# Optimization experiments

Hardware: AMD Instinct MI355X
Metric: run time of the kernel (lower is better)

The kernel has to match this reference:

```python
import jax, jax.numpy as jnp
import numpy as np

BITS = 8
EPS = 1e-5


def round_clip(x, lo, hi):
    # round-then-clip with straight-through estimator (matches Audyn's round_clip)
    return x + jax.lax.stop_gradient(jnp.clip(jnp.round(x), lo, hi) - x)


def setup_inputs() -> dict:
    key = jax.random.key(0)
    kx, kw = jax.random.split(key)
    B, S, D_IN, D_OUT = 4, 2048, 4096, 16384
    x = jax.random.normal(kx, (B, S, D_IN), dtype=jnp.float32)
    # kaiming-uniform-ish scale: bound = 1/sqrt(in_features)
    bound = 1.0 / np.sqrt(D_IN)
    weight = jax.random.uniform(kw, (D_OUT, D_IN), dtype=jnp.float32,
                                minval=-bound, maxval=bound)
    return {"x": x, "weight": weight}


def reference(x, weight):
    q = float(2 ** (BITS - 1))  # 128
    # activation quantization: per-tensor abs-max
    gamma = jnp.maximum(jnp.max(jnp.abs(x)), EPS)
    xq = round_clip(x * (q / gamma), -q, q - 1.0)
    # weight quantization: per-tensor mean-abs (NB: source divides abs_weight, not weight)
    abs_w = jnp.abs(weight)
    beta = jnp.maximum(jnp.mean(abs_w), EPS)
    wq = round_clip(abs_w / beta, -1.0, 1.0)
    # GEMM (no bias: source always registers bias as None) + rescale
    y = jnp.einsum("bsd,od->bso", xq, wq)
    return y * (beta * gamma / q)
```

## Files before the change

### kernel.cpp

```cpp
#include <hip/hip_runtime.h>

typedef float f32x4 __attribute__((ext_vector_type(4)));
typedef int   i32x4 __attribute__((ext_vector_type(4)));
typedef char  s8x16 __attribute__((ext_vector_type(16)));

#define GAS __attribute__((address_space(1)))
#define LAS __attribute__((address_space(3)))

constexpr int M = 8192;
constexpr int N = 16384;
constexpr int K = 4096;
constexpr long long NX = (long long)M * K;
constexpr long long NW = (long long)N * K;
constexpr int NPART = 2048;


__global__ void reduce_absmax_kernel(const float* __restrict__ x,
                                     unsigned* __restrict__ gmax, int n4) {
  float m = 0.f;
  int stride = gridDim.x * blockDim.x;
  for (int i = blockIdx.x * blockDim.x + threadIdx.x; i < n4; i += stride) {
    f32x4 v = *(const f32x4*)(x + (size_t)i * 4);
    m = fmaxf(m, fmaxf(fmaxf(fabsf(v[0]), fabsf(v[1])),
                       fmaxf(fabsf(v[2]), fabsf(v[3]))));
  }
#pragma unroll
  for (int off = 32; off > 0; off >>= 1) m = fmaxf(m, __shfl_down(m, off));
  __shared__ float sm[4];
  int lane = threadIdx.x & 63, wid = threadIdx.x >> 6;
  if (lane == 0) sm[wid] = m;
  __syncthreads();
  if (threadIdx.x == 0) {
    m = fmaxf(fmaxf(sm[0], sm[1]), fmaxf(sm[2], sm[3]));
    atomicMax(gmax, __float_as_uint(m));
  }
}

__global__ void reduce_abssum_kernel(const float* __restrict__ w,
                                     float* __restrict__ partials, int n4) {
  float s = 0.f;
  int stride = gridDim.x * blockDim.x;
  for (int i = blockIdx.x * blockDim.x + threadIdx.x; i < n4; i += stride) {
    f32x4 v = *(const f32x4*)(w + (size_t)i * 4);
    s += fabsf(v[0]) + fabsf(v[1]) + fabsf(v[2]) + fabsf(v[3]);
  }
#pragma unroll
  for (int off = 32; off > 0; off >>= 1) s += __shfl_down(s, off);
  __shared__ float sm[4];
  int lane = threadIdx.x & 63, wid = threadIdx.x >> 6;
  if (lane == 0) sm[wid] = s;
  __syncthreads();
  if (threadIdx.x == 0) partials[blockIdx.x] = (sm[0] + sm[1]) + (sm[2] + sm[3]);
}

__global__ void finalize_kernel(const unsigned* __restrict__ gbits,
                                const float* __restrict__ partials,
                                float* __restrict__ params) {
  __shared__ double sd[256];
  double s = 0.0;
  for (int i = threadIdx.x; i < NPART; i += 256) s += (double)partials[i];
  sd[threadIdx.x] = s;
  __syncthreads();
  for (int h = 128; h > 0; h >>= 1) {
    if (threadIdx.x < h) sd[threadIdx.x] += sd[threadIdx.x + h];
    __syncthreads();
  }
  if (threadIdx.x == 0) {
    float beta  = fmaxf((float)(sd[0] / (double)NW), 1e-5f);
    float gamma = fmaxf(__uint_as_float(gbits[0]), 1e-5f);
    params[0] = 128.0f / gamma;
    params[1] = beta;
    params[2] = beta * gamma / 128.0f;
  }
}


__global__ void quant_x_kernel(const float* __restrict__ x,
                               char* __restrict__ xq,
                               const float* __restrict__ params, int n16) {
  float s = params[0];
  int stride = gridDim.x * blockDim.x;
  for (int i = blockIdx.x * blockDim.x + threadIdx.x; i < n16; i += stride) {
    const f32x4* p = (const f32x4*)(x + (size_t)i * 16);
    s8x16 o;
#pragma unroll
    for (int v = 0; v < 4; ++v) {
      f32x4 t = p[v];
#pragma unroll
      for (int k = 0; k < 4; ++k) {
        float r = fminf(fmaxf(rintf(t[k] * s), -128.f), 127.f);
        o[v * 4 + k] = (char)(int)r;
      }
    }
    *(s8x16*)(xq + (size_t)i * 16) = o;
  }
}

__global__ void quant_w_kernel(const float* __restrict__ w,
                               char* __restrict__ wq,
                               const float* __restrict__ params, int n16) {
  float beta = params[1];
  int stride = gridDim.x * blockDim.x;
  for (int i = blockIdx.x * blockDim.x + threadIdx.x; i < n16; i += stride) {
    const f32x4* p = (const f32x4*)(w + (size_t)i * 16);
    s8x16 o;
#pragma unroll
    for (int v = 0; v < 4; ++v) {
      f32x4 t = p[v];
#pragma unroll
      for (int k = 0; k < 4; ++k) {
        o[v * 4 + k] = (rintf(fabsf(t[k]) / beta) >= 1.0f) ? (char)1 : (char)0;
      }
    }
    *(s8x16*)(wq + (size_t)i * 16) = o;
  }
}


__global__ __launch_bounds__(256) void gemm_kernel(
    const char* __restrict__ A,
    const char* __restrict__ B,
    float* __restrict__ C,
    const float* __restrict__ params) {
  __shared__ __align__(16) char As[128 * 64];
  __shared__ __align__(16) char Bs[128 * 64];

  const int tid  = threadIdx.x;
  const int lane = tid & 63, wid = tid >> 6;
  const int wr = wid >> 1, wc = wid & 1;
  const int r16 = lane & 15, q4 = lane >> 4;
  const int m0 = blockIdx.y * 128, n0 = blockIdx.x * 128;
  const float sc = params[2];

  const int i0 = tid, i1 = 256 + tid;
  const char* ga0 = A + (size_t)(m0 + (i0 >> 2)) * K + (i0 & 3) * 16;
  const char* ga1 = A + (size_t)(m0 + (i1 >> 2)) * K + (i1 & 3) * 16;
  const char* gb0 = B + (size_t)(n0 + (i0 >> 2)) * K + (i0 & 3) * 16;
  const char* gb1 = B + (size_t)(n0 + (i1 >> 2)) * K + (i1 & 3) * 16;
  char* la0 = &As[i0 * 16];
  char* la1 = &As[i1 * 16];
  char* lb0 = &Bs[i0 * 16];
  char* lb1 = &Bs[i1 * 16];

  int aoff[4], boff[4];
#pragma unroll
  for (int i = 0; i < 4; ++i) {
    aoff[i] = (wr * 64 + i * 16 + r16) * 64 + q4 * 16;
    boff[i] = (wc * 64 + i * 16 + r16) * 64 + q4 * 16;
  }

  i32x4 acc[4][4] = {};

  for (int kt = 0; kt < K / 64; ++kt) {
    const int ko = kt * 64;
    __builtin_amdgcn_global_load_lds((const GAS void*)(ga0 + ko), (LAS void*)la0, 16, 0, 0);
    __builtin_amdgcn_global_load_lds((const GAS void*)(ga1 + ko), (LAS void*)la1, 16, 0, 0);
    __builtin_amdgcn_global_load_lds((const GAS void*)(gb0 + ko), (LAS void*)lb0, 16, 0, 0);
    __builtin_amdgcn_global_load_lds((const GAS void*)(gb1 + ko), (LAS void*)lb1, 16, 0, 0);
    __syncthreads();

    i32x4 af[4], bf[4];
#pragma unroll
    for (int i = 0; i < 4; ++i) af[i] = *(const i32x4*)&As[aoff[i]];
#pragma unroll
    for (int j = 0; j < 4; ++j) bf[j] = *(const i32x4*)&Bs[boff[j]];
#pragma unroll
    for (int i = 0; i < 4; ++i)
#pragma unroll
      for (int j = 0; j < 4; ++j)
        acc[i][j] = __builtin_amdgcn_mfma_i32_16x16x64_i8(af[i], bf[j], acc[i][j], 0, 0, 0);
    __syncthreads();
  }

  const int crow = m0 + wr * 64 + q4 * 4;
  const int ccol = n0 + wc * 64 + r16;
#pragma unroll
  for (int i = 0; i < 4; ++i)
#pragma unroll
    for (int j = 0; j < 4; ++j)
#pragma unroll
      for (int r = 0; r < 4; ++r)
        C[(size_t)(crow + i * 16 + r) * N + (ccol + j * 16)] = (float)acc[i][j][r] * sc;
}


extern "C" void kernel_launch(void* const* d_in, const int* in_sizes, int n_in,
                              void* d_out, int out_size, void* d_ws, size_t ws_size,
                              hipStream_t stream) {
  const float* x = (const float*)d_in[0];
  const float* w = (const float*)d_in[1];
  float* out = (float*)d_out;
  char* ws = (char*)d_ws;

  unsigned* gamma_bits = (unsigned*)ws;
  float*    params     = (float*)(ws + 16);
  float*    partials   = (float*)(ws + 256);
  char*     xq = ws + 16384;
  char*     wq = ws + 16384 + (size_t)NX;

  hipMemsetAsync(ws, 0, 256, stream);

  reduce_absmax_kernel<<<NPART, 256, 0, stream>>>(x, gamma_bits, (int)(NX / 4));
  reduce_abssum_kernel<<<NPART, 256, 0, stream>>>(w, partials, (int)(NW / 4));
  finalize_kernel<<<1, 256, 0, stream>>>(gamma_bits, partials, params);
  quant_x_kernel<<<2048, 256, 0, stream>>>(x, xq, params, (int)(NX / 16));
  quant_w_kernel<<<2048, 256, 0, stream>>>(w, wq, params, (int)(NW / 16));

  dim3 grid(N / 128, M / 128);
  gemm_kernel<<<grid, 256, 0, stream>>>(xq, wq, out, params);
}
```

Measured before the change: 863.4 us.

## Triple-buffer GEMM LDS tiles with swizzled layout and async prefetch

The int8 GEMM main loop now uses a three-stage LDS ring buffer. Global-to-LDS loads for tile k+2 are issued before computing tile k, and each iteration uses one barrier gated by a partial vmcnt wait instead of two full syncthreads. The LDS layout gets an XOR swizzle on 16-byte columns to reduce bank conflicts on fragment reads, and MFMA issue priority is raised during compute. The cost is three times the LDS footprint (48KB per block), which may lower occupancy, and the correctness of the hand-written waitcnt sequencing becomes a risk.

```diff
diff --git a/kernel.cpp b/kernel.cpp
--- a/kernel.cpp
+++ b/kernel.cpp
@@ -13,6 +13,10 @@
 constexpr long long NX = (long long)M * K;
 constexpr long long NW = (long long)N * K;
 constexpr int NPART = 2048;
+constexpr int BK = 64;
+constexpr int NT = K / BK;
+constexpr int OP_BYTES = 128 * BK;
+constexpr int BUF_BYTES = 2 * OP_BYTES;
 
 
 __global__ void reduce_absmax_kernel(const float* __restrict__ x,
@@ -122,56 +126,88 @@
     const char* __restrict__ B,
     float* __restrict__ C,
     const float* __restrict__ params) {
-  __shared__ __align__(16) char As[128 * 64];
-  __shared__ __align__(16) char Bs[128 * 64];
+  __shared__ __align__(16) char lds[3 * BUF_BYTES];
 
   const int tid  = threadIdx.x;
   const int lane = tid & 63, wid = tid >> 6;
   const int wr = wid >> 1, wc = wid & 1;
   const int r16 = lane & 15, q4 = lane >> 4;
   const int m0 = blockIdx.y * 128, n0 = blockIdx.x * 128;
-  const float sc = params[2];
 
   const int i0 = tid, i1 = 256 + tid;
-  const char* ga0 = A + (size_t)(m0 + (i0 >> 2)) * K + (i0 & 3) * 16;
-  const char* ga1 = A + (size_t)(m0 + (i1 >> 2)) * K + (i1 & 3) * 16;
-  const char* gb0 = B + (size_t)(n0 + (i0 >> 2)) * K + (i0 & 3) * 16;
-  const char* gb1 = B + (size_t)(n0 + (i1 >> 2)) * K + (i1 & 3) * 16;
-  char* la0 = &As[i0 * 16];
-  char* la1 = &As[i1 * 16];
-  char* lb0 = &Bs[i0 * 16];
-  char* lb1 = &Bs[i1 * 16];
+  const int row0 = i0 >> 2, row1 = i1 >> 2;
+  const int c0 = ((i0 & 3) * 16) ^ (((row0 >> 1) & 3) << 4);
+  const int c1 = ((i1 & 3) * 16) ^ (((row1 >> 1) & 3) << 4);
+  const char* ga0 = A + (size_t)(m0 + row0) * K + c0;
+  const char* ga1 = A + (size_t)(m0 + row1) * K + c1;
+  const char* gb0 = B + (size_t)(n0 + row0) * K + c0;
+  const char* gb1 = B + (size_t)(n0 + row1) * K + c1;
 
   int aoff[4], boff[4];
 #pragma unroll
   for (int i = 0; i < 4; ++i) {
-    aoff[i] = (wr * 64 + i * 16 + r16) * 64 + q4 * 16;
-    boff[i] = (wc * 64 + i * 16 + r16) * 64 + q4 * 16;
+    const int sw = (q4 * 16) ^ (((r16 >> 1) & 3) << 4);
+    aoff[i] = (wr * 64 + i * 16 + r16) * BK + sw;
+    boff[i] = (wc * 64 + i * 16 + r16) * BK + sw;
   }
 
   i32x4 acc[4][4] = {};
 
-  for (int kt = 0; kt < K / 64; ++kt) {
-    const int ko = kt * 64;
-    __builtin_amdgcn_global_load_lds((const GAS void*)(ga0 + ko), (LAS void*)la0, 16, 0, 0);
-    __builtin_amdgcn_global_load_lds((const GAS void*)(ga1 + ko), (LAS void*)la1, 16, 0, 0);
-    __builtin_amdgcn_global_load_lds((const GAS void*)(gb0 + ko), (LAS void*)lb0, 16, 0, 0);
-    __builtin_amdgcn_global_load_lds((const GAS void*)(gb1 + ko), (LAS void*)lb1, 16, 0, 0);
-    __syncthreads();
-
+  auto stage = [&](int t, int buf) {
+    char* la = lds + buf * BUF_BYTES;
+    char* lb = la + OP_BYTES;
+    const int ko = t * BK;
+    __builtin_amdgcn_global_load_lds((const GAS void*)(ga0 + ko), (LAS void*)(la + i0 * 16), 16, 0, 0);
+    __builtin_amdgcn_global_load_lds((const GAS void*)(ga1 + ko), (LAS void*)(la + i1 * 16), 16, 0, 0);
+    __builtin_amdgcn_global_load_lds((const GAS void*)(gb0 + ko), (LAS void*)(lb + i0 * 16), 16, 0, 0);
+    __builtin_amdgcn_global_load_lds((const GAS void*)(gb1 + ko), (LAS void*)(lb + i1 * 16), 16, 0, 0);
+  };
+
+  auto compute = [&](int buf) {
+    const char* la = lds + buf * BUF_BYTES;
+    const char* lb = la + OP_BYTES;
     i32x4 af[4], bf[4];
 #pragma unroll
-    for (int i = 0; i < 4; ++i) af[i] = *(const i32x4*)&As[aoff[i]];
-#pragma unroll
-    for (int j = 0; j < 4; ++j) bf[j] = *(const i32x4*)&Bs[boff[j]];
+    for (int i = 0; i < 4; ++i) af[i] = *(const i32x4*)(la + aoff[i]);
+#pragma unroll
+    for (int j = 0; j < 4; ++j) bf[j] = *(const i32x4*)(lb + boff[j]);
+    __builtin_amdgcn_s_setprio(1);
 #pragma unroll
     for (int i = 0; i < 4; ++i)
 #pragma unroll
       for (int j = 0; j < 4; ++j)
         acc[i][j] = __builtin_amdgcn_mfma_i32_16x16x64_i8(af[i], bf[j], acc[i][j], 0, 0, 0);
-    __syncthreads();
-  }
-
+    __builtin_amdgcn_s_setprio(0);
+  };
+
+  stage(0, 0);
+  stage(1, 1);
+
+  int cb = 0;
+  int sb = 2;
+  for (int kt = 0; kt < NT - 2; ++kt) {
+    asm volatile("s_waitcnt vmcnt(4)" ::: "memory");
+    __builtin_amdgcn_sched_barrier(0);
+    __builtin_amdgcn_s_barrier();
+    __builtin_amdgcn_sched_barrier(0);
+    stage(kt + 2, sb);
+    compute(cb);
+    cb = (cb == 2) ? 0 : cb + 1;
+    sb = (sb == 2) ? 0 : sb + 1;
+  }
+  asm volatile("s_waitcnt vmcnt(4)" ::: "memory");
+  __builtin_amdgcn_sched_barrier(0);
+  __builtin_amdgcn_s_barrier();
+  __builtin_amdgcn_sched_barrier(0);
+  compute(cb);
+  cb = (cb == 2) ? 0 : cb + 1;
+  asm volatile("s_waitcnt vmcnt(0)" ::: "memory");
+  __builtin_amdgcn_sched_barrier(0);
+  __builtin_amdgcn_s_barrier();
+  __builtin_amdgcn_sched_barrier(0);
+  compute(cb);
+
+  const float sc = params[2];
   const int crow = m0 + wr * 64 + q4 * 4;
   const int ccol = n0 + wc * 64 + r16;
 #pragma unroll
```

Result: faster. 842.5 us (-2.4%).

## Rewrite int8 GEMM with 256x256 tiles, double-buffered swizzled LDS and grid remap

Applied to the files above, without the earlier changes.

Replaces the 128x128, 4-wave GEMM with a 256x256 tile computed by 8 waves. It uses a K-step of 128 and double-buffered 64KB LDS stages filled by global_load_lds. Loads of the next stage are issued before the MFMAs on the current one. An XOR chunk swizzle avoids LDS bank conflicts, and a block-index remap groups tiles for L2 reuse. The kernel also raises MFMA priority with setprio and adds extra barriers. The aim is less global traffic per flop and hidden load latency, in exchange for 128KB of LDS per block, which limits occupancy to one block per CU, plus high accumulator register pressure.

```diff
diff --git a/kernel.cpp b/kernel.cpp
--- a/kernel.cpp
+++ b/kernel.cpp
@@ -117,70 +117,120 @@
 }
 
 
-__global__ __launch_bounds__(256) void gemm_kernel(
+__global__ __launch_bounds__(512, 2) void gemm_kernel(
     const char* __restrict__ A,
     const char* __restrict__ B,
     float* __restrict__ C,
     const float* __restrict__ params) {
-  __shared__ __align__(16) char As[128 * 64];
-  __shared__ __align__(16) char Bs[128 * 64];
+  __shared__ __align__(16) char lds[131072];
 
   const int tid  = threadIdx.x;
   const int lane = tid & 63, wid = tid >> 6;
-  const int wr = wid >> 1, wc = wid & 1;
+  const int wm = wid >> 2, wn = wid & 3;
   const int r16 = lane & 15, q4 = lane >> 4;
-  const int m0 = blockIdx.y * 128, n0 = blockIdx.x * 128;
+
+  const int wg = (blockIdx.x & 7) * 256 + (blockIdx.x >> 3);
+  const int m0 = (wg >> 6) * 256, n0 = (wg & 63) * 256;
+
+  const int l8 = lane >> 3;
+  const int cswz = ((lane & 7) ^ l8) * 16;
+  const char* Ar = A + (size_t)(m0 + wid * 16 + l8) * K + cswz;
+  const char* Br = B + (size_t)(n0 + wid * 16 + l8) * K + cswz;
+  const int dbase = wid * 2048 + lane * 16;
+
+  auto stage = [&](int t, int b) {
+    char* L = lds + b * 65536;
+    const char* a0 = Ar + t * 128;
+    const char* b0 = Br + t * 128;
+    __builtin_amdgcn_global_load_lds((const GAS void*)(a0),               (LAS void*)(L + dbase),                16, 0, 0);
+    __builtin_amdgcn_global_load_lds((const GAS void*)(a0 + 8 * K),       (LAS void*)(L + dbase + 1024),         16, 0, 0);
+    __builtin_amdgcn_global_load_lds((const GAS void*)(a0 + 128 * K),     (LAS void*)(L + dbase + 16384),        16, 0, 0);
+    __builtin_amdgcn_global_load_lds((const GAS void*)(a0 + 136 * K),     (LAS void*)(L + dbase + 17408),        16, 0, 0);
+    __builtin_amdgcn_global_load_lds((const GAS void*)(b0),               (LAS void*)(L + dbase + 32768),        16, 0, 0);
+    __builtin_amdgcn_global_load_lds((const GAS void*)(b0 + 8 * K),       (LAS void*)(L + dbase + 33792),        16, 0, 0);
+    __builtin_amdgcn_global_load_lds((const GAS void*)(b0 + 128 * K),     (LAS void*)(L + dbase + 49152),        16, 0, 0);
+    __builtin_amdgcn_global_load_lds((const GAS void*)(b0 + 136 * K),     (LAS void*)(L + dbase + 50176),        16, 0, 0);
+  };
+
+  int aoff[8][2], boff[4][2];
+#pragma unroll
+  for (int i = 0; i < 8; ++i)
+#pragma unroll
+    for (int kh = 0; kh < 2; ++kh)
+      aoff[i][kh] = (wm * 128 + i * 16 + r16) * 128 + (((kh * 4 + q4) ^ (r16 & 7)) * 16);
+#pragma unroll
+  for (int j = 0; j < 4; ++j)
+#pragma unroll
+    for (int kh = 0; kh < 2; ++kh)
+      boff[j][kh] = 32768 + (wn * 64 + j * 16 + r16) * 128 + (((kh * 4 + q4) ^ (r16 & 7)) * 16);
+
+  i32x4 acc[8][4] = {};
+  i32x4 afr[8], bfr0, bfr1;
+
+  stage(0, 0);
+
+  for (int t = 0; t < 32; ++t) {
+    const char* buf = lds + (t & 1) * 65536;
+    asm volatile("s_waitcnt vmcnt(0)" ::: "memory");
+    __builtin_amdgcn_sched_barrier(0);
+    __builtin_amdgcn_s_barrier();
+    __builtin_amdgcn_sched_barrier(0);
+    if (t + 1 < 32) stage(t + 1, (t + 1) & 1);
+#pragma unroll
+    for (int i = 0; i < 8; ++i) afr[i] = *(const i32x4*)(buf + aoff[i][0]);
+    bfr0 = *(const i32x4*)(buf + boff[0][0]);
+    bfr1 = *(const i32x4*)(buf + boff[1][0]);
+    __builtin_amdgcn_s_setprio(1);
+#pragma unroll
+    for (int i = 0; i < 8; ++i) {
+      acc[i][0] = __builtin_amdgcn_mfma_i32_16x16x64_i8(afr[i], bfr0, acc[i][0], 0, 0, 0);
+      acc[i][1] = __builtin_amdgcn_mfma_i32_16x16x64_i8(afr[i], bfr1, acc[i][1], 0, 0, 0);
+    }
+    __builtin_amdgcn_s_setprio(0);
+    __builtin_amdgcn_s_barrier();
+    bfr0 = *(const i32x4*)(buf + boff[2][0]);
+    bfr1 = *(const i32x4*)(buf + boff[3][0]);
+    __builtin_amdgcn_s_setprio(1);
+#pragma unroll
+    for (int i = 0; i < 8; ++i) {
+      acc[i][2] = __builtin_amdgcn_mfma_i32_16x16x64_i8(afr[i], bfr0, acc[i][2], 0, 0, 0);
+      acc[i][3] = __builtin_amdgcn_mfma_i32_16x16x64_i8(afr[i], bfr1, acc[i][3], 0, 0, 0);
+    }
+    __builtin_amdgcn_s_setprio(0);
+    __builtin_amdgcn_s_barrier();
+#pragma unroll
+    for (int i = 0; i < 8; ++i) afr[i] = *(const i32x4*)(buf + aoff[i][1]);
+    bfr0 = *(const i32x4*)(buf + boff[0][1]);
+    bfr1 = *(const i32x4*)(buf + boff[1][1]);
+    __builtin_amdgcn_s_setprio(1);
+#pragma unroll
+    for (int i = 0; i < 8; ++i) {
+      acc[i][0] = __builtin_amdgcn_mfma_i32_16x16x64_i8(afr[i], bfr0, acc[i][0], 0, 0, 0);
+      acc[i][1] = __builtin_amdgcn_mfma_i32_16x16x64_i8(afr[i], bfr1, acc[i][1], 0, 0, 0);
+    }
+    __builtin_amdgcn_s_setprio(0);
+    __builtin_amdgcn_s_barrier();
+    bfr0 = *(const i32x4*)(buf + boff[2][1]);
+    bfr1 = *(const i32x4*)(buf + boff[3][1]);
+    __builtin_amdgcn_s_setprio(1);
+#pragma unroll
+    for (int i = 0; i < 8; ++i) {
+      acc[i][2] = __builtin_amdgcn_mfma_i32_16x16x64_i8(afr[i], bfr0, acc[i][2], 0, 0, 0);
+      acc[i][3] = __builtin_amdgcn_mfma_i32_16x16x64_i8(afr[i], bfr1, acc[i][3], 0, 0, 0);
+    }
+    __builtin_amdgcn_s_setprio(0);
+  }
+
   const float sc = params[2];
-
-  const int i0 = tid, i1 = 256 + tid;
-  const char* ga0 = A + (size_t)(m0 + (i0 >> 2)) * K + (i0 & 3) * 16;
-  const char* ga1 = A + (size_t)(m0 + (i1 >> 2)) * K + (i1 & 3) * 16;
-  const char* gb0 = B + (size_t)(n0 + (i0 >> 2)) * K + (i0 & 3) * 16;
-  const char* gb1 = B + (size_t)(n0 + (i1 >> 2)) * K + (i1 & 3) * 16;
-  char* la0 = &As[i0 * 16];
-  char* la1 = &As[i1 * 16];
-  char* lb0 = &Bs[i0 * 16];
-  char* lb1 = &Bs[i1 * 16];
-
-  int aoff[4], boff[4];
-#pragma unroll
-  for (int i = 0; i < 4; ++i) {
-    aoff[i] = (wr * 64 + i * 16 + r16) * 64 + q4 * 16;
-    boff[i] = (wc * 64 + i * 16 + r16) * 64 + q4 * 16;
-  }
-
-  i32x4 acc[4][4] = {};
-
-  for (int kt = 0; kt < K / 64; ++kt) {
-    const int ko = kt * 64;
-    __builtin_amdgcn_global_load_lds((const GAS void*)(ga0 + ko), (LAS void*)la0, 16, 0, 0);
-    __builtin_amdgcn_global_load_lds((const GAS void*)(ga1 + ko), (LAS void*)la1, 16, 0, 0);
-    __builtin_amdgcn_global_load_lds((const GAS void*)(gb0 + ko), (LAS void*)lb0, 16, 0, 0);
-    __builtin_amdgcn_global_load_lds((const GAS void*)(gb1 + ko), (LAS void*)lb1, 16, 0, 0);
-    __syncthreads();
-
-    i32x4 af[4], bf[4];
-#pragma unroll
-    for (int i = 0; i < 4; ++i) af[i] = *(const i32x4*)&As[aoff[i]];
-#pragma unroll
-    for (int j = 0; j < 4; ++j) bf[j] = *(const i32x4*)&Bs[boff[j]];
-#pragma unroll
-    for (int i = 0; i < 4; ++i)
-#pragma unroll
-      for (int j = 0; j < 4; ++j)
-        acc[i][j] = __builtin_amdgcn_mfma_i32_16x16x64_i8(af[i], bf[j], acc[i][j], 0, 0, 0);
-    __syncthreads();
-  }
-
-  const int crow = m0 + wr * 64 + q4 * 4;
-  const int ccol = n0 + wc * 64 + r16;
-#pragma unroll
-  for (int i = 0; i < 4; ++i)
-#pragma unroll
-    for (int j = 0; j < 4; ++j)
+  const int crow = m0 + wm * 128 + q4 * 4;
+  const int ccol = n0 + wn * 64 + r16;
+#pragma unroll
+  for (int i = 0; i < 8; ++i)
+#pragma unroll
+    for (int jj = 0; jj < 4; ++jj)
 #pragma unroll
       for (int r = 0; r < 4; ++r)
-        C[(size_t)(crow + i * 16 + r) * N + (ccol + j * 16)] = (float)acc[i][j][r] * sc;
+        C[(size_t)(crow + i * 16 + r) * N + (ccol + jj * 16)] = (float)acc[i][jj][r] * sc;
 }
 
 
@@ -206,6 +256,5 @@
   quant_x_kernel<<<2048, 256, 0, stream>>>(x, xq, params, (int)(NX / 16));
   quant_w_kernel<<<2048, 256, 0, stream>>>(w, wq, params, (int)(NW / 16));
 
-  dim3 grid(N / 128, M / 128);
-  gemm_kernel<<<grid, 256, 0, stream>>>(xq, wq, out, params);
-}
+  gemm_kernel<<<2048, 512, 0, stream>>>(xq, wq, out, params);
+}
```

Result: faster. 765.2 us (-11.4%).

## Triple-buffer int8 GEMM with 256x128 tiles, swizzled LDS, and block remap

Applied to the files above, without the earlier changes.

Rewrites the int8 MFMA GEMM to use 512-thread blocks computing 256x128 tiles, with a three-stage LDS ring of global_load_lds prefetches. This lets loads for tile t+2 overlap compute on tile t, replacing the old load-sync-compute-sync loop. It also XOR-swizzles LDS columns to cut bank conflicts, remaps block IDs to group neighboring tiles for L2 reuse, and raises MFMA issue priority with setprio. In exchange it needs more LDS per block and relies on a hand-written vmcnt count that must match the number of outstanding loads.

```diff
diff --git a/kernel.cpp b/kernel.cpp
--- a/kernel.cpp
+++ b/kernel.cpp
@@ -13,6 +13,12 @@
 constexpr long long NX = (long long)M * K;
 constexpr long long NW = (long long)N * K;
 constexpr int NPART = 2048;
+
+constexpr int BKB    = 64;
+constexpr int NTT    = K / BKB;
+constexpr int ABYTES = 256 * BKB;
+constexpr int BBYTES = 128 * BKB;
+constexpr int BUFB   = ABYTES + BBYTES;
 
 
 __global__ void reduce_absmax_kernel(const float* __restrict__ x,
@@ -117,63 +123,85 @@
 }
 
 
-__global__ __launch_bounds__(256) void gemm_kernel(
+__global__ __launch_bounds__(512, 4) void gemm_kernel(
     const char* __restrict__ A,
     const char* __restrict__ B,
     float* __restrict__ C,
     const float* __restrict__ params) {
-  __shared__ __align__(16) char As[128 * 64];
-  __shared__ __align__(16) char Bs[128 * 64];
+  __shared__ __align__(16) char lds[3 * BUFB];
 
   const int tid  = threadIdx.x;
   const int lane = tid & 63, wid = tid >> 6;
-  const int wr = wid >> 1, wc = wid & 1;
+  const int wm = wid >> 1, wn = wid & 1;
   const int r16 = lane & 15, q4 = lane >> 4;
-  const int m0 = blockIdx.y * 128, n0 = blockIdx.x * 128;
-  const float sc = params[2];
-
-  const int i0 = tid, i1 = 256 + tid;
-  const char* ga0 = A + (size_t)(m0 + (i0 >> 2)) * K + (i0 & 3) * 16;
-  const char* ga1 = A + (size_t)(m0 + (i1 >> 2)) * K + (i1 & 3) * 16;
-  const char* gb0 = B + (size_t)(n0 + (i0 >> 2)) * K + (i0 & 3) * 16;
-  const char* gb1 = B + (size_t)(n0 + (i1 >> 2)) * K + (i1 & 3) * 16;
-  char* la0 = &As[i0 * 16];
-  char* la1 = &As[i1 * 16];
-  char* lb0 = &Bs[i0 * 16];
-  char* lb1 = &Bs[i1 * 16];
+
+  const int wg = (blockIdx.x & 7) * 512 + (blockIdx.x >> 3);
+  const int m0 = (wg >> 7) * 256, n0 = (wg & 127) * 128;
+
+  const int csw = (((lane & 3) ^ ((lane >> 3) & 3))) * 16;
+  const char* gA = A + (size_t)(m0 + wid * 32 + (lane >> 2)) * K + csw;
+  const char* gB = B + (size_t)(n0 + wid * 16 + (lane >> 2)) * K + csw;
+  const int dA = wid * 2048 + lane * 16;
+  const int dB = ABYTES + wid * 1024 + lane * 16;
+
+  auto stage = [&](int t, int bo) {
+    char* L = lds + bo;
+    const char* a = gA + t * BKB;
+    __builtin_amdgcn_global_load_lds((const GAS void*)a,              (LAS void*)(L + dA),        16, 0, 0);
+    __builtin_amdgcn_global_load_lds((const GAS void*)(a + 16 * K),   (LAS void*)(L + dA + 1024), 16, 0, 0);
+    __builtin_amdgcn_global_load_lds((const GAS void*)(gB + t * BKB), (LAS void*)(L + dB),        16, 0, 0);
+  };
 
   int aoff[4], boff[4];
-#pragma unroll
-  for (int i = 0; i < 4; ++i) {
-    aoff[i] = (wr * 64 + i * 16 + r16) * 64 + q4 * 16;
-    boff[i] = (wc * 64 + i * 16 + r16) * 64 + q4 * 16;
-  }
+  const int rsw = ((q4 ^ ((r16 >> 1) & 3)) * 16);
+#pragma unroll
+  for (int i = 0; i < 4; ++i)
+    aoff[i] = (wm * 64 + i * 16 + r16) * BKB + rsw;
+#pragma unroll
+  for (int j = 0; j < 4; ++j)
+    boff[j] = ABYTES + (wn * 64 + j * 16 + r16) * BKB + rsw;
 
   i32x4 acc[4][4] = {};
 
-  for (int kt = 0; kt < K / 64; ++kt) {
-    const int ko = kt * 64;
-    __builtin_amdgcn_global_load_lds((const GAS void*)(ga0 + ko), (LAS void*)la0, 16, 0, 0);
-    __builtin_amdgcn_global_load_lds((const GAS void*)(ga1 + ko), (LAS void*)la1, 16, 0, 0);
-    __builtin_amdgcn_global_load_lds((const GAS void*)(gb0 + ko), (LAS void*)lb0, 16, 0, 0);
-    __builtin_amdgcn_global_load_lds((const GAS void*)(gb1 + ko), (LAS void*)lb1, 16, 0, 0);
-    __syncthreads();
-
+  auto compute = [&](int bo) {
+    const char* buf = lds + bo;
     i32x4 af[4], bf[4];
 #pragma unroll
-    for (int i = 0; i < 4; ++i) af[i] = *(const i32x4*)&As[aoff[i]];
-#pragma unroll
-    for (int j = 0; j < 4; ++j) bf[j] = *(const i32x4*)&Bs[boff[j]];
+    for (int i = 0; i < 4; ++i) af[i] = *(const i32x4*)(buf + aoff[i]);
+#pragma unroll
+    for (int j = 0; j < 4; ++j) bf[j] = *(const i32x4*)(buf + boff[j]);
+    __builtin_amdgcn_s_setprio(1);
 #pragma unroll
     for (int i = 0; i < 4; ++i)
 #pragma unroll
       for (int j = 0; j < 4; ++j)
         acc[i][j] = __builtin_amdgcn_mfma_i32_16x16x64_i8(af[i], bf[j], acc[i][j], 0, 0, 0);
-    __syncthreads();
-  }
-
-  const int crow = m0 + wr * 64 + q4 * 4;
-  const int ccol = n0 + wc * 64 + r16;
+    __builtin_amdgcn_s_setprio(0);
+  };
+
+  stage(0, 0);
+  stage(1, BUFB);
+
+  int cb = 0, sb = 2 * BUFB;
+  for (int t = 0; t < NTT - 1; ++t) {
+    asm volatile("s_waitcnt vmcnt(3)" ::: "memory");
+    __builtin_amdgcn_sched_barrier(0);
+    __builtin_amdgcn_s_barrier();
+    __builtin_amdgcn_sched_barrier(0);
+    if (t + 2 < NTT) stage(t + 2, sb);
+    compute(cb);
+    cb = (cb == 2 * BUFB) ? 0 : cb + BUFB;
+    sb = (sb == 2 * BUFB) ? 0 : sb + BUFB;
+  }
+  asm volatile("s_waitcnt vmcnt(0)" ::: "memory");
+  __builtin_amdgcn_sched_barrier(0);
+  __builtin_amdgcn_s_barrier();
+  __builtin_amdgcn_sched_barrier(0);
+  compute(cb);
+
+  const float sc = params[2];
+  const int crow = m0 + wm * 64 + q4 * 4;
+  const int ccol = n0 + wn * 64 + r16;
 #pragma unroll
   for (int i = 0; i < 4; ++i)
 #pragma unroll
@@ -206,6 +234,5 @@
   quant_x_kernel<<<2048, 256, 0, stream>>>(x, xq, params, (int)(NX / 16));
   quant_w_kernel<<<2048, 256, 0, stream>>>(w, wq, params, (int)(NW / 16));
 
-  dim3 grid(N / 128, M / 128);
-  gemm_kernel<<<grid, 256, 0, stream>>>(xq, wq, out, params);
-}
+  gemm_kernel<<<4096, 512, 0, stream>>>(xq, wq, out, params);
+}
```

Measured after the change: 756.3 us. 12.4% less time.
